# Optimization experiments

Hardware: AMD Instinct MI355X
Metric: run time of the kernel (lower is better)

The kernel has to match this reference:

```python
import jax, jax.numpy as jnp
import numpy as np

GRID_SIZE = 3
LN_EPS = 1e-5
BASIS_EPS = 1e-6


def setup_inputs() -> dict:
    key = jax.random.key(0)
    ks = jax.random.split(key, 5)
    B, S, D_IN, D_OUT, SE_H = 8, 1024, 1024, 1024, 32
    x = jax.random.normal(ks[0], (B, S, D_IN), dtype=jnp.float32)
    base_weight = jax.random.normal(ks[1], (D_OUT, D_IN), dtype=jnp.float32) * 0.01
    spline_weight = jax.random.normal(ks[2], (D_OUT, D_IN, GRID_SIZE), dtype=jnp.float32) * 0.005
    ln_w = jnp.ones((D_OUT,), dtype=jnp.float32)
    ln_b = jnp.zeros((D_OUT,), dtype=jnp.float32)
    se_w1 = jax.random.normal(ks[3], (SE_H, D_OUT), dtype=jnp.float32) * 0.03
    se_b1 = jnp.zeros((SE_H,), dtype=jnp.float32)
    se_w2 = jax.random.normal(ks[4], (D_OUT, SE_H), dtype=jnp.float32) * 0.03
    se_b2 = jnp.zeros((D_OUT,), dtype=jnp.float32)
    return {"x": x, "base_weight": base_weight, "spline_weight": spline_weight,
            "ln_w": ln_w, "ln_b": ln_b, "se_w1": se_w1, "se_b1": se_b1,
            "se_w2": se_w2, "se_b2": se_b2}


def _kan_layer(x2d, base_weight, spline_weight, ln_w, ln_b, se_w1, se_b1, se_w2, se_b2):
    # x2d: [N, D_in]
    base = x2d @ base_weight.T                                   # [N, D_out]
    grid = jnp.linspace(-1.0, 1.0, GRID_SIZE).astype(x2d.dtype)  # [G]
    dist = jnp.abs(x2d[..., None] - grid)                        # [N, D_in, G]
    basis = jnp.where(dist < 1.0, (1.0 - dist) ** 2, 0.0)
    basis = basis / (basis.sum(axis=-1, keepdims=True) + BASIS_EPS)
    spline = jnp.einsum('nig,oig->no', basis, spline_weight)     # [N, D_out]
    out = base + spline
    # LayerNorm (dropout is identity at inference)
    mu = out.mean(axis=-1, keepdims=True)
    var = ((out - mu) ** 2).mean(axis=-1, keepdims=True)
    out = (out - mu) * jax.lax.rsqrt(var + LN_EPS) * ln_w + ln_b
    # SE gating (2D branch: applied per flattened token)
    h = jnp.maximum(out @ se_w1.T + se_b1, 0.0)
    se = jax.nn.sigmoid(h @ se_w2.T + se_b2)
    return out * se


def reference(x, base_weight, spline_weight, ln_w, ln_b, se_w1, se_b1, se_w2, se_b2):
    B, S, D = x.shape
    out = _kan_layer(x.reshape(-1, D), base_weight, spline_weight,
                     ln_w, ln_b, se_w1, se_b1, se_w2, se_b2)
    return out.reshape(B, S, -1)
```

## Files before the change

### kernel.cpp

```cpp
#include <hip/hip_runtime.h>
#include <hip/hip_bf16.h>
#include <math.h>

typedef __attribute__((ext_vector_type(8))) __bf16 bf16x8;
typedef __attribute__((ext_vector_type(4))) float f32x4;

#define NTOK 8192
#define DIN 1024
#define DOUT 1024
#define KAUG 4096
#define SEH 32

#define BK 64
#define NKT (KAUG / BK)

static __device__ __forceinline__ unsigned short f2bf(float f) {
  union { float f; unsigned u; } v; v.f = f;
  unsigned r = (v.u + 0x7FFFu + ((v.u >> 16) & 1u)) >> 16;
  return (unsigned short)r;
}

__global__ __launch_bounds__(256) void prep(const float* __restrict__ x,
                                            const float* __restrict__ bw,
                                            const float* __restrict__ sw,
                                            const float* __restrict__ w1,
                                            const float* __restrict__ w2,
                                            ushort* __restrict__ Aaug,
                                            ushort* __restrict__ Waug,
                                            ushort* __restrict__ w1b,
                                            ushort* __restrict__ w2b) {
  const int b = blockIdx.x;
  if (b < 32768) {
    const int id = b * 256 + threadIdx.x;
    const float v = x[id];
    const float d0 = fabsf(v + 1.f), d1 = fabsf(v), d2 = fabsf(v - 1.f);
    float b0 = (d0 < 1.f) ? (1.f - d0) * (1.f - d0) : 0.f;
    float b1 = (d1 < 1.f) ? (1.f - d1) * (1.f - d1) : 0.f;
    float b2 = (d2 < 1.f) ? (1.f - d2) * (1.f - d2) : 0.f;
    const float inv = 1.f / (b0 + b1 + b2 + 1e-6f);
    ushort4 o;
    o.x = f2bf(v);
    o.y = f2bf(b0 * inv);
    o.z = f2bf(b1 * inv);
    o.w = f2bf(b2 * inv);
    ((ushort4*)Aaug)[id] = o;
  } else if (b < 32768 + 4096) {
    const int id = (b - 32768) * 256 + threadIdx.x;
    ushort4 o;
    o.x = f2bf(bw[id]);
    o.y = f2bf(sw[id * 3 + 0]);
    o.z = f2bf(sw[id * 3 + 1]);
    o.w = f2bf(sw[id * 3 + 2]);
    ((ushort4*)Waug)[id] = o;
  } else {
    const int id = (b - 32768 - 4096) * 256 + threadIdx.x;
    if (id < SEH * DOUT) w1b[id] = f2bf(w1[id]);
    else w2b[id - SEH * DOUT] = f2bf(w2[id - SEH * DOUT]);
  }
}

#define WAITVM(N) asm volatile("s_waitcnt vmcnt(" #N ")" ::: "memory")

__global__ __launch_bounds__(256, 2) void gemm_ns(const ushort* __restrict__ A,
                                                  const ushort* __restrict__ B,
                                                  float* __restrict__ C) {
  __shared__ ushort As[2][128 * BK];
  __shared__ ushort Bs[2][128 * BK];
  const int tid = threadIdx.x;
  const int wid = tid >> 6, lane = tid & 63;
  const int l16 = lane & 15, lk = lane >> 4;
  const int wm = wid >> 1, wn = wid & 1;

  const int g = (blockIdx.x & 7) * 64 + (blockIdx.x >> 3);
  const int bm = g >> 3;
  const int bn = g & 7;

  const ushort* Ab = A + (size_t)bm * 128 * KAUG;
  const ushort* Bb = B + (size_t)bn * 128 * KAUG;

  const int lrow = lane >> 3;
  const int lcb = (lane & 7) ^ lrow;

  const int aBase = (wm * 64 + l16) * 64;
  const int bBase = (wn * 64 + l16) * 64;
  const int sw0 = ((l16 & 4) << 3) + ((lk ^ (l16 & 3)) << 3);
  const int sw1 = sw0 ^ 32;

  f32x4 acc[4][4] = {};

#define STAGE_A(kt, buf, r)                                                     \
  __builtin_amdgcn_global_load_lds(                                             \
      (const __attribute__((address_space(1))) void*)(Ab +                      \
          (size_t)((r) * 32 + wid * 8 + lrow) * KAUG + (kt) * BK + lcb * 8),    \
      (__attribute__((address_space(3))) void*)(&As[buf][((r) * 256 + wid * 64) * 8]), \
      16, 0, 0)
#define STAGE_B(kt, buf, r)                                                     \
  __builtin_amdgcn_global_load_lds(                                             \
      (const __attribute__((address_space(1))) void*)(Bb +                      \
          (size_t)((r) * 32 + wid * 8 + lrow) * KAUG + (kt) * BK + lcb * 8),    \
      (__attribute__((address_space(3))) void*)(&Bs[buf][((r) * 256 + wid * 64) * 8]), \
      16, 0, 0)
#define STAGE_ALL(kt, buf)                                                      \
  do {                                                                          \
    STAGE_A(kt, buf, 0); STAGE_A(kt, buf, 1); STAGE_A(kt, buf, 2); STAGE_A(kt, buf, 3); \
    STAGE_B(kt, buf, 0); STAGE_B(kt, buf, 1); STAGE_B(kt, buf, 2); STAGE_B(kt, buf, 3); \
  } while (0)

#define TILE(kt, CB, NB)                                                        \
  do {                                                                          \
    if ((kt) < NKT - 1) {                                                       \
      STAGE_ALL((kt) + 1, NB);                                                  \
      WAITVM(8);                                                                \
    } else {                                                                    \
      WAITVM(0);                                                                \
    }                                                                           \
    __builtin_amdgcn_s_barrier();                                               \
    __builtin_amdgcn_sched_barrier(0);                                          \
    bf16x8 af[4][2], bfr[4][2];                                                 \
    _Pragma("unroll")                                                           \
    for (int m = 0; m < 4; ++m) {                                               \
      af[m][0] = *(const bf16x8*)&As[CB][aBase + m * 1024 + sw0];               \
      af[m][1] = *(const bf16x8*)&As[CB][aBase + m * 1024 + sw1];               \
    }                                                                           \
    _Pragma("unroll")                                                           \
    for (int n = 0; n < 4; ++n) {                                               \
      bfr[n][0] = *(const bf16x8*)&Bs[CB][bBase + n * 1024 + sw0];              \
      bfr[n][1] = *(const bf16x8*)&Bs[CB][bBase + n * 1024 + sw1];              \
    }                                                                           \
    __builtin_amdgcn_s_setprio(1);                                              \
    _Pragma("unroll")                                                           \
    for (int k2 = 0; k2 < 2; ++k2)                                              \
      _Pragma("unroll")                                                         \
      for (int m = 0; m < 4; ++m)                                               \
        _Pragma("unroll")                                                       \
        for (int n = 0; n < 4; ++n)                                             \
          acc[m][n] = __builtin_amdgcn_mfma_f32_16x16x32_bf16(                  \
              af[m][k2], bfr[n][k2], acc[m][n], 0, 0, 0);                       \
    __builtin_amdgcn_s_setprio(0);                                              \
    __builtin_amdgcn_s_barrier();                                               \
  } while (0)

  STAGE_ALL(0, 0);

  for (int kt2 = 0; kt2 < NKT; kt2 += 2) {
    TILE(kt2, 0, 1);
    TILE(kt2 + 1, 1, 0);
  }

  float* Cb = C + (size_t)(bm * 128 + wm * 64) * DOUT + bn * 128 + wn * 64;
#pragma unroll
  for (int m = 0; m < 4; ++m)
#pragma unroll
    for (int n = 0; n < 4; ++n)
#pragma unroll
      for (int j = 0; j < 4; ++j)
        Cb[(size_t)(m * 16 + lk * 4 + j) * DOUT + n * 16 + l16] = acc[m][n][j];
}

__global__ __launch_bounds__(256) void ln_se_mfma(
    float* __restrict__ out,
    const float* __restrict__ ln_w, const float* __restrict__ ln_b,
    const ushort* __restrict__ w1b, const float* __restrict__ se_b1,
    const ushort* __restrict__ w2b, const float* __restrict__ se_b2) {
  __shared__ float Yl[16 * 1028];
  __shared__ float Hpart[4][512];
  __shared__ unsigned Hb[256];
  const int tid = threadIdx.x;
  const int w = tid >> 6, lane = tid & 63;
  const int l16 = lane & 15, lk = lane >> 4;
  const int tok0 = blockIdx.x * 16;

  float lw[16], lb[16];
#pragma unroll
  for (int e = 0; e < 16; ++e) {
    lw[e] = ln_w[e * 64 + lane];
    lb[e] = ln_b[e * 64 + lane];
  }

  for (int q = 0; q < 4; ++q) {
    const int tl = w * 4 + q;
    const float* r0 = out + (size_t)(tok0 + tl) * DOUT;
    float v[16];
#pragma unroll
    for (int e = 0; e < 16; ++e) v[e] = r0[e * 64 + lane];
    float s = 0.f, ss = 0.f;
#pragma unroll
    for (int e = 0; e < 16; ++e) { s += v[e]; ss += v[e] * v[e]; }
#pragma unroll
    for (int m = 32; m; m >>= 1) { s += __shfl_xor(s, m); ss += __shfl_xor(ss, m); }
    const float mu = s * (1.f / (float)DOUT);
    const float inv = rsqrtf(ss * (1.f / (float)DOUT) - mu * mu + 1e-5f);
#pragma unroll
    for (int e = 0; e < 16; ++e)
      Yl[tl * 1028 + e * 64 + lane] = (v[e] - mu) * inv * lw[e] + lb[e];
  }
  __syncthreads();

  f32x4 acc1[2] = {};
#pragma unroll
  for (int s = 0; s < 8; ++s) {
    const int ks = w * 8 + s;
    const int k = ks * 32 + lk * 8;
    const float* yp = &Yl[l16 * 1028 + k];
    const f32x4 q0 = *(const f32x4*)yp;
    const f32x4 q1 = *(const f32x4*)(yp + 4);
    bf16x8 af;
    af[0] = (__bf16)q0[0]; af[1] = (__bf16)q0[1];
    af[2] = (__bf16)q0[2]; af[3] = (__bf16)q0[3];
    af[4] = (__bf16)q1[0]; af[5] = (__bf16)q1[1];
    af[6] = (__bf16)q1[2]; af[7] = (__bf16)q1[3];
#pragma unroll
    for (int nt = 0; nt < 2; ++nt) {
      const bf16x8 bf = *(const bf16x8*)(w1b + (nt * 16 + l16) * 1024 + ks * 32 + lk * 8);
      acc1[nt] = __builtin_amdgcn_mfma_f32_16x16x32_bf16(af, bf, acc1[nt], 0, 0, 0);
    }
  }
#pragma unroll
  for (int nt = 0; nt < 2; ++nt)
#pragma unroll
    for (int j = 0; j < 4; ++j)
      Hpart[w][(lk * 4 + j) * 32 + nt * 16 + l16] = acc1[nt][j];
  __syncthreads();

  {
    const int e2 = tid * 2;
    float h0 = Hpart[0][e2] + Hpart[1][e2] + Hpart[2][e2] + Hpart[3][e2];
    float h1 = Hpart[0][e2 + 1] + Hpart[1][e2 + 1] + Hpart[2][e2 + 1] + Hpart[3][e2 + 1];
    h0 = fmaxf(h0 + se_b1[e2 & 31], 0.f);
    h1 = fmaxf(h1 + se_b1[(e2 & 31) + 1], 0.f);
    Hb[tid] = (unsigned)f2bf(h0) | ((unsigned)f2bf(h1) << 16);
  }
  __syncthreads();

  union { uint4 u; bf16x8 v; } ha;
  ha.u = *(const uint4*)&Hb[l16 * 16 + lk * 4];
  const int nbase = w * 256;
#pragma unroll
  for (int nt = 0; nt < 16; ++nt) {
    const int col = nbase + nt * 16 + l16;
    const bf16x8 bf = *(const bf16x8*)(w2b + col * 32 + lk * 8);
    f32x4 gz = {0.f, 0.f, 0.f, 0.f};
    gz = __builtin_amdgcn_mfma_f32_16x16x32_bf16(ha.v, bf, gz, 0, 0, 0);
    const float b2 = se_b2[col];
#pragma unroll
    for (int j = 0; j < 4; ++j) {
      const int tl = lk * 4 + j;
      const float sg = 1.f / (1.f + __expf(-(gz[j] + b2)));
      out[(size_t)(tok0 + tl) * DOUT + col] = Yl[tl * 1028 + col] * sg;
    }
  }
}

extern "C" void kernel_launch(void* const* d_in, const int* in_sizes, int n_in,
                              void* d_out, int out_size, void* d_ws, size_t ws_size,
                              hipStream_t stream) {
  const float* x = (const float*)d_in[0];
  const float* bw = (const float*)d_in[1];
  const float* sw = (const float*)d_in[2];
  const float* ln_w = (const float*)d_in[3];
  const float* ln_b = (const float*)d_in[4];
  const float* se_w1 = (const float*)d_in[5];
  const float* se_b1 = (const float*)d_in[6];
  const float* se_w2 = (const float*)d_in[7];
  const float* se_b2 = (const float*)d_in[8];
  float* out = (float*)d_out;

  ushort* Aaug = (ushort*)d_ws;
  ushort* Waug = Aaug + (size_t)NTOK * KAUG;
  ushort* w1b = Waug + (size_t)DOUT * KAUG;
  ushort* w2b = w1b + SEH * DOUT;

  prep<<<32768 + 4096 + 256, 256, 0, stream>>>(x, bw, sw, se_w1, se_w2,
                                               Aaug, Waug, w1b, w2b);
  gemm_ns<<<512, 256, 0, stream>>>(Aaug, Waug, out);
  ln_se_mfma<<<NTOK / 16, 256, 0, stream>>>(out, ln_w, ln_b,
                                            w1b, se_b1, w2b, se_b2);
}
```

Measured before the change: 108.3 us.

## Split GEMM K dimension in two and sum partials in LayerNorm kernel

Measured after the change: 124.8 us. 1.15x slower.

```diff
diff --git a/kernel.cpp b/kernel.cpp
--- a/kernel.cpp
+++ b/kernel.cpp
@@ -11,8 +11,9 @@
 #define KAUG 4096
 #define SEH 32
 
-#define BK 64
-#define NKT (KAUG / BK)
+#define KHALF 2048
+#define BK32 32
+#define NKT2 (KHALF / BK32)
 
 static __device__ __forceinline__ unsigned short f2bf(float f) {
   union { float f; unsigned u; } v; v.f = f;
@@ -61,93 +62,86 @@
 
 #define WAITVM(N) asm volatile("s_waitcnt vmcnt(" #N ")" ::: "memory")
 
-__global__ __launch_bounds__(256, 2) void gemm_ns(const ushort* __restrict__ A,
-                                                  const ushort* __restrict__ B,
-                                                  float* __restrict__ C) {
-  __shared__ ushort As[2][128 * BK];
-  __shared__ ushort Bs[2][128 * BK];
+__global__ __launch_bounds__(256, 4) void gemm_sk32(const ushort* __restrict__ A,
+                                                    const ushort* __restrict__ B,
+                                                    float* __restrict__ P0,
+                                                    float* __restrict__ P1) {
+  __shared__ ushort As[2][128 * BK32];
+  __shared__ ushort Bs[2][128 * BK32];
   const int tid = threadIdx.x;
   const int wid = tid >> 6, lane = tid & 63;
   const int l16 = lane & 15, lk = lane >> 4;
   const int wm = wid >> 1, wn = wid & 1;
 
-  const int g = (blockIdx.x & 7) * 64 + (blockIdx.x >> 3);
-  const int bm = g >> 3;
+  const int g = (blockIdx.x & 7) * 128 + (blockIdx.x >> 3);
+  const int kh = g >> 9;
+  const int bm = (g >> 3) & 63;
   const int bn = g & 7;
 
-  const ushort* Ab = A + (size_t)bm * 128 * KAUG;
-  const ushort* Bb = B + (size_t)bn * 128 * KAUG;
-
-  const int lrow = lane >> 3;
-  const int lcb = (lane & 7) ^ lrow;
-
-  const int aBase = (wm * 64 + l16) * 64;
-  const int bBase = (wn * 64 + l16) * 64;
-  const int sw0 = ((l16 & 4) << 3) + ((lk ^ (l16 & 3)) << 3);
-  const int sw1 = sw0 ^ 32;
+  const ushort* Ab = A + (size_t)bm * 128 * KAUG + kh * KHALF;
+  const ushort* Bb = B + (size_t)bn * 128 * KAUG + kh * KHALF;
+  float* P = kh ? P1 : P0;
+
+  const int srow = lane >> 2;
+  const int scol = (lane & 3) ^ ((lane >> 3) & 3);
+
+  const int aBase = (wm * 64 + l16) * 32 + ((lk ^ ((l16 >> 1) & 3)) << 3);
+  const int bBase = (wn * 64 + l16) * 32 + ((lk ^ ((l16 >> 1) & 3)) << 3);
 
   f32x4 acc[4][4] = {};
 
-#define STAGE_A(kt, buf, r)                                                     \
+#define STAGE_A32(kt, buf, r)                                                   \
   __builtin_amdgcn_global_load_lds(                                             \
       (const __attribute__((address_space(1))) void*)(Ab +                      \
-          (size_t)((r) * 32 + wid * 8 + lrow) * KAUG + (kt) * BK + lcb * 8),    \
+          (size_t)((r) * 64 + wid * 16 + srow) * KAUG + (kt) * BK32 + scol * 8),\
       (__attribute__((address_space(3))) void*)(&As[buf][((r) * 256 + wid * 64) * 8]), \
       16, 0, 0)
-#define STAGE_B(kt, buf, r)                                                     \
+#define STAGE_B32(kt, buf, r)                                                   \
   __builtin_amdgcn_global_load_lds(                                             \
       (const __attribute__((address_space(1))) void*)(Bb +                      \
-          (size_t)((r) * 32 + wid * 8 + lrow) * KAUG + (kt) * BK + lcb * 8),    \
+          (size_t)((r) * 64 + wid * 16 + srow) * KAUG + (kt) * BK32 + scol * 8),\
       (__attribute__((address_space(3))) void*)(&Bs[buf][((r) * 256 + wid * 64) * 8]), \
       16, 0, 0)
-#define STAGE_ALL(kt, buf)                                                      \
+#define STAGE_ALL32(kt, buf)                                                    \
   do {                                                                          \
-    STAGE_A(kt, buf, 0); STAGE_A(kt, buf, 1); STAGE_A(kt, buf, 2); STAGE_A(kt, buf, 3); \
-    STAGE_B(kt, buf, 0); STAGE_B(kt, buf, 1); STAGE_B(kt, buf, 2); STAGE_B(kt, buf, 3); \
+    STAGE_A32(kt, buf, 0); STAGE_A32(kt, buf, 1);                               \
+    STAGE_B32(kt, buf, 0); STAGE_B32(kt, buf, 1);                               \
   } while (0)
 
-#define TILE(kt, CB, NB)                                                        \
+#define TILE32(kt, CB, NB)                                                      \
   do {                                                                          \
-    if ((kt) < NKT - 1) {                                                       \
-      STAGE_ALL((kt) + 1, NB);                                                  \
-      WAITVM(8);                                                                \
+    if ((kt) < NKT2 - 1) {                                                      \
+      STAGE_ALL32((kt) + 1, NB);                                                \
+      WAITVM(4);                                                                \
     } else {                                                                    \
       WAITVM(0);                                                                \
     }                                                                           \
     __builtin_amdgcn_s_barrier();                                               \
     __builtin_amdgcn_sched_barrier(0);                                          \
-    bf16x8 af[4][2], bfr[4][2];                                                 \
+    bf16x8 af[4], bfr[4];                                                       \
     _Pragma("unroll")                                                           \
-    for (int m = 0; m < 4; ++m) {                                               \
-      af[m][0] = *(const bf16x8*)&As[CB][aBase + m * 1024 + sw0];               \
-      af[m][1] = *(const bf16x8*)&As[CB][aBase + m * 1024 + sw1];               \
-    }                                                                           \
+    for (int m = 0; m < 4; ++m) af[m] = *(const bf16x8*)&As[CB][aBase + m * 512]; \
     _Pragma("unroll")                                                           \
-    for (int n = 0; n < 4; ++n) {                                               \
-      bfr[n][0] = *(const bf16x8*)&Bs[CB][bBase + n * 1024 + sw0];              \
-      bfr[n][1] = *(const bf16x8*)&Bs[CB][bBase + n * 1024 + sw1];              \
-    }                                                                           \
+    for (int n = 0; n < 4; ++n) bfr[n] = *(const bf16x8*)&Bs[CB][bBase + n * 512]; \
     __builtin_amdgcn_s_setprio(1);                                              \
     _Pragma("unroll")                                                           \
-    for (int k2 = 0; k2 < 2; ++k2)                                              \
+    for (int m = 0; m < 4; ++m)                                                 \
       _Pragma("unroll")                                                         \
-      for (int m = 0; m < 4; ++m)                                               \
-        _Pragma("unroll")                                                       \
-        for (int n = 0; n < 4; ++n)                                             \
-          acc[m][n] = __builtin_amdgcn_mfma_f32_16x16x32_bf16(                  \
-              af[m][k2], bfr[n][k2], acc[m][n], 0, 0, 0);                       \
+      for (int n = 0; n < 4; ++n)                                               \
+        acc[m][n] = __builtin_amdgcn_mfma_f32_16x16x32_bf16(                    \
+            af[m], bfr[n], acc[m][n], 0, 0, 0);                                 \
     __builtin_amdgcn_s_setprio(0);                                              \
     __builtin_amdgcn_s_barrier();                                               \
   } while (0)
 
-  STAGE_ALL(0, 0);
-
-  for (int kt2 = 0; kt2 < NKT; kt2 += 2) {
-    TILE(kt2, 0, 1);
-    TILE(kt2 + 1, 1, 0);
-  }
-
-  float* Cb = C + (size_t)(bm * 128 + wm * 64) * DOUT + bn * 128 + wn * 64;
+  STAGE_ALL32(0, 0);
+
+  for (int kt2 = 0; kt2 < NKT2; kt2 += 2) {
+    TILE32(kt2, 0, 1);
+    TILE32(kt2 + 1, 1, 0);
+  }
+
+  float* Cb = P + (size_t)(bm * 128 + wm * 64) * DOUT + bn * 128 + wn * 64;
 #pragma unroll
   for (int m = 0; m < 4; ++m)
 #pragma unroll
@@ -158,7 +152,7 @@
 }
 
 __global__ __launch_bounds__(256) void ln_se_mfma(
-    float* __restrict__ out,
+    float* __restrict__ out, const float* __restrict__ p1,
     const float* __restrict__ ln_w, const float* __restrict__ ln_b,
     const ushort* __restrict__ w1b, const float* __restrict__ se_b1,
     const ushort* __restrict__ w2b, const float* __restrict__ se_b2) {
@@ -170,29 +164,43 @@
   const int l16 = lane & 15, lk = lane >> 4;
   const int tok0 = blockIdx.x * 16;
 
-  float lw[16], lb[16];
-#pragma unroll
-  for (int e = 0; e < 16; ++e) {
-    lw[e] = ln_w[e * 64 + lane];
-    lb[e] = ln_b[e * 64 + lane];
-  }
-
+  float4 lwv[4], lbv[4];
+#pragma unroll
   for (int q = 0; q < 4; ++q) {
-    const int tl = w * 4 + q;
-    const float* r0 = out + (size_t)(tok0 + tl) * DOUT;
-    float v[16];
-#pragma unroll
-    for (int e = 0; e < 16; ++e) v[e] = r0[e * 64 + lane];
+    lwv[q] = ((const float4*)ln_w)[q * 64 + lane];
+    lbv[q] = ((const float4*)ln_b)[q * 64 + lane];
+  }
+
+  for (int qt = 0; qt < 4; ++qt) {
+    const int tl = w * 4 + qt;
+    const float4* r0 = (const float4*)(out + (size_t)(tok0 + tl) * DOUT);
+    const float4* r1 = (const float4*)(p1 + (size_t)(tok0 + tl) * DOUT);
+    float4 v[4];
+#pragma unroll
+    for (int q = 0; q < 4; ++q) {
+      const float4 a = r0[q * 64 + lane], b = r1[q * 64 + lane];
+      v[q].x = a.x + b.x; v[q].y = a.y + b.y;
+      v[q].z = a.z + b.z; v[q].w = a.w + b.w;
+    }
     float s = 0.f, ss = 0.f;
 #pragma unroll
-    for (int e = 0; e < 16; ++e) { s += v[e]; ss += v[e] * v[e]; }
+    for (int q = 0; q < 4; ++q) {
+      s += v[q].x + v[q].y + v[q].z + v[q].w;
+      ss += v[q].x * v[q].x + v[q].y * v[q].y + v[q].z * v[q].z + v[q].w * v[q].w;
+    }
 #pragma unroll
     for (int m = 32; m; m >>= 1) { s += __shfl_xor(s, m); ss += __shfl_xor(ss, m); }
     const float mu = s * (1.f / (float)DOUT);
     const float inv = rsqrtf(ss * (1.f / (float)DOUT) - mu * mu + 1e-5f);
 #pragma unroll
-    for (int e = 0; e < 16; ++e)
-      Yl[tl * 1028 + e * 64 + lane] = (v[e] - mu) * inv * lw[e] + lb[e];
+    for (int q = 0; q < 4; ++q) {
+      float4 yv;
+      yv.x = (v[q].x - mu) * inv * lwv[q].x + lbv[q].x;
+      yv.y = (v[q].y - mu) * inv * lwv[q].y + lbv[q].y;
+      yv.z = (v[q].z - mu) * inv * lwv[q].z + lbv[q].z;
+      yv.w = (v[q].w - mu) * inv * lwv[q].w + lbv[q].w;
+      *(float4*)&Yl[tl * 1028 + (q * 64 + lane) * 4] = yv;
+    }
   }
   __syncthreads();
 
@@ -269,10 +277,11 @@
   ushort* Waug = Aaug + (size_t)NTOK * KAUG;
   ushort* w1b = Waug + (size_t)DOUT * KAUG;
   ushort* w2b = w1b + SEH * DOUT;
+  float* P1 = (float*)(w2b + SEH * DOUT);
 
   prep<<<32768 + 4096 + 256, 256, 0, stream>>>(x, bw, sw, se_w1, se_w2,
                                                Aaug, Waug, w1b, w2b);
-  gemm_ns<<<512, 256, 0, stream>>>(Aaug, Waug, out);
-  ln_se_mfma<<<NTOK / 16, 256, 0, stream>>>(out, ln_w, ln_b,
+  gemm_sk32<<<1024, 256, 0, stream>>>(Aaug, Waug, out, P1);
+  ln_se_mfma<<<NTOK / 16, 256, 0, stream>>>(out, P1, ln_w, ln_b,
                                             w1b, se_b1, w2b, se_b2);
 }
```

## Load GEMM B fragments directly to registers and vectorize LayerNorm loads

Applied to the files above, without the earlier changes.

New measurement: 181.5 us. +67.6%, slower.

```diff
diff --git a/kernel.cpp b/kernel.cpp
--- a/kernel.cpp
+++ b/kernel.cpp
@@ -65,7 +65,6 @@
                                                   const ushort* __restrict__ B,
                                                   float* __restrict__ C) {
   __shared__ ushort As[2][128 * BK];
-  __shared__ ushort Bs[2][128 * BK];
   const int tid = threadIdx.x;
   const int wid = tid >> 6, lane = tid & 63;
   const int l16 = lane & 15, lk = lane >> 4;
@@ -76,17 +75,17 @@
   const int bn = g & 7;
 
   const ushort* Ab = A + (size_t)bm * 128 * KAUG;
-  const ushort* Bb = B + (size_t)bn * 128 * KAUG;
+  const ushort* Bf0 = B + (size_t)(bn * 128 + wn * 64 + l16) * KAUG + lk * 8;
 
   const int lrow = lane >> 3;
   const int lcb = (lane & 7) ^ lrow;
 
   const int aBase = (wm * 64 + l16) * 64;
-  const int bBase = (wn * 64 + l16) * 64;
   const int sw0 = ((l16 & 4) << 3) + ((lk ^ (l16 & 3)) << 3);
   const int sw1 = sw0 ^ 32;
 
   f32x4 acc[4][4] = {};
+  bf16x8 bA[4][2], bB[4][2];
 
 #define STAGE_A(kt, buf, r)                                                     \
   __builtin_amdgcn_global_load_lds(                                             \
@@ -94,39 +93,35 @@
           (size_t)((r) * 32 + wid * 8 + lrow) * KAUG + (kt) * BK + lcb * 8),    \
       (__attribute__((address_space(3))) void*)(&As[buf][((r) * 256 + wid * 64) * 8]), \
       16, 0, 0)
-#define STAGE_B(kt, buf, r)                                                     \
-  __builtin_amdgcn_global_load_lds(                                             \
-      (const __attribute__((address_space(1))) void*)(Bb +                      \
-          (size_t)((r) * 32 + wid * 8 + lrow) * KAUG + (kt) * BK + lcb * 8),    \
-      (__attribute__((address_space(3))) void*)(&Bs[buf][((r) * 256 + wid * 64) * 8]), \
-      16, 0, 0)
-#define STAGE_ALL(kt, buf)                                                      \
+#define STAGE_A4(kt, buf)                                                       \
+  do { STAGE_A(kt, buf, 0); STAGE_A(kt, buf, 1); STAGE_A(kt, buf, 2); STAGE_A(kt, buf, 3); } while (0)
+
+#define BLOAD(dst, kt)                                                          \
   do {                                                                          \
-    STAGE_A(kt, buf, 0); STAGE_A(kt, buf, 1); STAGE_A(kt, buf, 2); STAGE_A(kt, buf, 3); \
-    STAGE_B(kt, buf, 0); STAGE_B(kt, buf, 1); STAGE_B(kt, buf, 2); STAGE_B(kt, buf, 3); \
+    _Pragma("unroll")                                                           \
+    for (int n = 0; n < 4; ++n) {                                               \
+      dst[n][0] = *(const bf16x8*)(Bf0 + (size_t)n * 16 * KAUG + (kt) * BK);    \
+      dst[n][1] = *(const bf16x8*)(Bf0 + (size_t)n * 16 * KAUG + (kt) * BK + 32); \
+    }                                                                           \
   } while (0)
 
-#define TILE(kt, CB, NB)                                                        \
+#define TILE(kt, CB, NB, BC, BNX)                                               \
   do {                                                                          \
     if ((kt) < NKT - 1) {                                                       \
-      STAGE_ALL((kt) + 1, NB);                                                  \
+      STAGE_A4((kt) + 1, NB);                                                   \
+      WAITVM(12);                                                               \
+    } else {                                                                    \
       WAITVM(8);                                                                \
-    } else {                                                                    \
-      WAITVM(0);                                                                \
     }                                                                           \
     __builtin_amdgcn_s_barrier();                                               \
     __builtin_amdgcn_sched_barrier(0);                                          \
-    bf16x8 af[4][2], bfr[4][2];                                                 \
+    bf16x8 af[4][2];                                                            \
     _Pragma("unroll")                                                           \
     for (int m = 0; m < 4; ++m) {                                               \
       af[m][0] = *(const bf16x8*)&As[CB][aBase + m * 1024 + sw0];               \
       af[m][1] = *(const bf16x8*)&As[CB][aBase + m * 1024 + sw1];               \
     }                                                                           \
-    _Pragma("unroll")                                                           \
-    for (int n = 0; n < 4; ++n) {                                               \
-      bfr[n][0] = *(const bf16x8*)&Bs[CB][bBase + n * 1024 + sw0];              \
-      bfr[n][1] = *(const bf16x8*)&Bs[CB][bBase + n * 1024 + sw1];              \
-    }                                                                           \
+    if ((kt) < NKT - 1) BLOAD(BNX, (kt) + 1);   \
     __builtin_amdgcn_s_setprio(1);                                              \
     _Pragma("unroll")                                                           \
     for (int k2 = 0; k2 < 2; ++k2)                                              \
@@ -135,16 +130,17 @@
         _Pragma("unroll")                                                       \
         for (int n = 0; n < 4; ++n)                                             \
           acc[m][n] = __builtin_amdgcn_mfma_f32_16x16x32_bf16(                  \
-              af[m][k2], bfr[n][k2], acc[m][n], 0, 0, 0);                       \
+              af[m][k2], BC[n][k2], acc[m][n], 0, 0, 0);                        \
     __builtin_amdgcn_s_setprio(0);                                              \
     __builtin_amdgcn_s_barrier();                                               \
   } while (0)
 
-  STAGE_ALL(0, 0);
+  STAGE_A4(0, 0);
+  BLOAD(bA, 0);
 
   for (int kt2 = 0; kt2 < NKT; kt2 += 2) {
-    TILE(kt2, 0, 1);
-    TILE(kt2 + 1, 1, 0);
+    TILE(kt2, 0, 1, bA, bB);
+    TILE(kt2 + 1, 1, 0, bB, bA);
   }
 
   float* Cb = C + (size_t)(bm * 128 + wm * 64) * DOUT + bn * 128 + wn * 64;
@@ -170,29 +166,38 @@
   const int l16 = lane & 15, lk = lane >> 4;
   const int tok0 = blockIdx.x * 16;
 
-  float lw[16], lb[16];
-#pragma unroll
-  for (int e = 0; e < 16; ++e) {
-    lw[e] = ln_w[e * 64 + lane];
-    lb[e] = ln_b[e * 64 + lane];
-  }
-
+  float4 lwv[4], lbv[4];
+#pragma unroll
   for (int q = 0; q < 4; ++q) {
-    const int tl = w * 4 + q;
-    const float* r0 = out + (size_t)(tok0 + tl) * DOUT;
-    float v[16];
-#pragma unroll
-    for (int e = 0; e < 16; ++e) v[e] = r0[e * 64 + lane];
+    lwv[q] = ((const float4*)ln_w)[q * 64 + lane];
+    lbv[q] = ((const float4*)ln_b)[q * 64 + lane];
+  }
+
+  for (int qt = 0; qt < 4; ++qt) {
+    const int tl = w * 4 + qt;
+    const float4* r0 = (const float4*)(out + (size_t)(tok0 + tl) * DOUT);
+    float4 v[4];
+#pragma unroll
+    for (int q = 0; q < 4; ++q) v[q] = r0[q * 64 + lane];
     float s = 0.f, ss = 0.f;
 #pragma unroll
-    for (int e = 0; e < 16; ++e) { s += v[e]; ss += v[e] * v[e]; }
+    for (int q = 0; q < 4; ++q) {
+      s += v[q].x + v[q].y + v[q].z + v[q].w;
+      ss += v[q].x * v[q].x + v[q].y * v[q].y + v[q].z * v[q].z + v[q].w * v[q].w;
+    }
 #pragma unroll
     for (int m = 32; m; m >>= 1) { s += __shfl_xor(s, m); ss += __shfl_xor(ss, m); }
     const float mu = s * (1.f / (float)DOUT);
     const float inv = rsqrtf(ss * (1.f / (float)DOUT) - mu * mu + 1e-5f);
 #pragma unroll
-    for (int e = 0; e < 16; ++e)
-      Yl[tl * 1028 + e * 64 + lane] = (v[e] - mu) * inv * lw[e] + lb[e];
+    for (int q = 0; q < 4; ++q) {
+      float4 yv;
+      yv.x = (v[q].x - mu) * inv * lwv[q].x + lbv[q].x;
+      yv.y = (v[q].y - mu) * inv * lwv[q].y + lbv[q].y;
+      yv.z = (v[q].z - mu) * inv * lwv[q].z + lbv[q].z;
+      yv.w = (v[q].w - mu) * inv * lwv[q].w + lbv[q].w;
+      *(float4*)&Yl[tl * 1028 + (q * 64 + lane) * 4] = yv;
+    }
   }
   __syncthreads();
 
```
